# Kernel tuning notes

Measured on AMD Instinct MI355X. Metric: run time of the kernel, lower is better.

The kernel has to match this reference:

```python
import jax, jax.numpy as jnp
import numpy as np
from jax import lax

M = 512      # num_centers
K = 32       # neighbors per center
FEAT = 256   # token feature dim
EPS = 1e-5   # BatchNorm eps


def fps(xyz, m):
    """Furthest point sampling. xyz: (B,N,3) -> idx (B,m) int32."""
    B, N, _ = xyz.shape
    first = jnp.zeros((B,), jnp.int32)

    def step(carry, _):
        min_d, last = carry                       # (B,N), (B,)
        last_pt = jnp.take_along_axis(xyz, last[:, None, None], axis=1)  # (B,1,3)
        d = jnp.sum((xyz - last_pt) ** 2, axis=-1)                       # (B,N)
        min_d = jnp.minimum(min_d, d)
        nxt = jnp.argmax(min_d, axis=1).astype(jnp.int32)
        return (min_d, nxt), nxt

    init = (jnp.full((B, N), 1e10, jnp.float32), first)
    _, rest = lax.scan(step, init, None, length=m - 1)   # (m-1, B)
    return jnp.concatenate([first[None, :], rest], axis=0).T  # (B,m)


def bn(x, g, b, mean, var):
    return (x - mean) * (g * lax.rsqrt(var + EPS)) + b


def setup_inputs() -> dict:
    key = jax.random.key(0)
    ks = jax.random.split(key, 16)
    B, N = 8, 16384
    r = lambda k_, s, sc=0.1: jax.random.normal(k_, s, jnp.float32) * sc
    inp = {
        "xyz": jax.random.normal(ks[0], (B, N, 3), jnp.float32),
        "W1": r(ks[1], (64, 3)), "b1": r(ks[2], (64,)),
        "g1": 1.0 + r(ks[3], (64,)), "be1": r(ks[4], (64,)),
        "m1": r(ks[5], (64,)), "v1": 1.0 + 0.1 * jax.random.uniform(ks[6], (64,)),
        "W2": r(ks[7], (128, 64)), "b2": r(ks[8], (128,)),
        "g2": 1.0 + r(ks[9], (128,)), "be2": r(ks[10], (128,)),
        "m2": r(ks[11], (128,)), "v2": 1.0 + 0.1 * jax.random.uniform(ks[12], (128,)),
        "W3": r(ks[13], (FEAT, 128)), "b3": r(ks[14], (FEAT,)),
        "Wp": r(ks[15], (FEAT, 3)), "bp": jnp.zeros((FEAT,), jnp.float32),
    }
    return inp


def reference(xyz, W1, b1, g1, be1, m1, v1, W2, b2, g2, be2, m2, v2, W3, b3, Wp, bp):
    B, N, _ = xyz.shape
    # --- FPS centers ---
    idx_c = fps(xyz, M)                                            # (B,M)
    centers = jnp.take_along_axis(xyz, idx_c[:, :, None], axis=1)  # (B,M,3)
    # --- brute-force KNN ---
    dist = jnp.sum((centers[:, :, None, :] - xyz[:, None, :, :]) ** 2, axis=-1)  # (B,M,N)
    _, idx = lax.top_k(-dist, K)                                   # (B,M,K)
    nbrs = jnp.take_along_axis(
        xyz, idx.reshape(B, M * K)[:, :, None], axis=1
    ).reshape(B, M, K, 3)
    grouped = nbrs - centers[:, :, None, :]                        # (B,M,K,3)
    # --- MiniPointNet: 1x1 convs == channel matmuls, eval-mode BN ---
    h = jnp.einsum("bmkc,oc->bmko", grouped, W1) + b1
    h = jax.nn.relu(bn(h, g1, be1, m1, v1))
    h = jnp.einsum("bmkc,oc->bmko", h, W2) + b2
    h = jax.nn.relu(bn(h, g2, be2, m2, v2))
    h = jnp.einsum("bmkc,oc->bmko", h, W3) + b3
    tokens = jnp.max(h, axis=2)                                    # (B,M,FEAT)
    pos = jnp.einsum("bmc,oc->bmo", centers, Wp) + bp
    return centers, tokens + pos
```

## Files before the change

### kernel.cpp

```cpp
#include <hip/hip_runtime.h>

typedef unsigned int u32;
typedef unsigned long long u64;
typedef unsigned short u16;

#define DEVFN static __device__ __forceinline__

constexpr int NPTS = 16384;
constexpr int NC = 512;

typedef __attribute__((ext_vector_type(8))) short bf16x8;
typedef __attribute__((ext_vector_type(4))) float f32x4;

#define MFMA16(a, b, c) __builtin_amdgcn_mfma_f32_16x16x32_bf16(a, b, c, 0, 0, 0)

DEVFN u16 bf16rne(float f) {
  u32 b = __float_as_uint(f);
  u32 r = (b + 0x7FFFu + ((b >> 16) & 1u)) >> 16;
  return (u16)r;
}

DEVFN u64 shflx64(u64 v, int m) {
  u32 lo = __shfl_xor((u32)v, m, 64);
  u32 hi = __shfl_xor((u32)(v >> 32), m, 64);
  return ((u64)hi << 32) | lo;
}
DEVFN u64 shfl64(u64 v, int src) {
  u32 lo = __shfl((u32)v, src, 64);
  u32 hi = __shfl((u32)(v >> 32), src, 64);
  return ((u64)hi << 32) | lo;
}

DEVFN void csw(u64& a, u64& b) {
  u64 lo = a < b ? a : b;
  u64 hi = a < b ? b : a;
  a = lo; b = hi;
}

DEVFN u32 spread3(u32 v) {
  return (v & 1u) | ((v & 2u) << 2) | ((v & 4u) << 4) | ((v & 8u) << 6);
}

__global__ __launch_bounds__(1024, 4) void fps_kernel(const float* __restrict__ xyz,
                                                      float* __restrict__ centers) {
  const int b = blockIdx.x;
  const int t = threadIdx.x;
  const int lane = t & 63;
  const int w = t >> 6;
  const float* xb = xyz + (size_t)b * NPTS * 3;

  __shared__ char smem[86016];
  u32* hist = (u32*)smem;
  u16* soidx = (u16*)(smem + 8192);
  u64* skeybuf = (u64*)(smem + 40960);
  float* redB = (float*)(smem + 41216);
  u32* redW = (u32*)(smem + 41664);

  const u32 inf10 = __float_as_uint(1e10f);

  u32 mcode[16];
  {
    float ox[16], oy[16], oz[16];
    float lx = 1e30f, ly = 1e30f, lz = 1e30f;
    float hx = -1e30f, hy = -1e30f, hz = -1e30f;
#pragma unroll
    for (int j = 0; j < 16; ++j) {
      int p = t + j * 1024;
      ox[j] = xb[p * 3 + 0];
      oy[j] = xb[p * 3 + 1];
      oz[j] = xb[p * 3 + 2];
      lx = fminf(lx, ox[j]); hx = fmaxf(hx, ox[j]);
      ly = fminf(ly, oy[j]); hy = fmaxf(hy, oy[j]);
      lz = fminf(lz, oz[j]); hz = fmaxf(hz, oz[j]);
    }
#pragma unroll
    for (int s = 32; s; s >>= 1) {
      lx = fminf(lx, __shfl_xor(lx, s, 64)); hx = fmaxf(hx, __shfl_xor(hx, s, 64));
      ly = fminf(ly, __shfl_xor(ly, s, 64)); hy = fmaxf(hy, __shfl_xor(hy, s, 64));
      lz = fminf(lz, __shfl_xor(lz, s, 64)); hz = fmaxf(hz, __shfl_xor(hz, s, 64));
    }
    if (lane == 0) {
      redB[w * 6 + 0] = lx; redB[w * 6 + 1] = hx;
      redB[w * 6 + 2] = ly; redB[w * 6 + 3] = hy;
      redB[w * 6 + 4] = lz; redB[w * 6 + 5] = hz;
    }
    hist[t] = 0; hist[t + 1024] = 0;
    __syncthreads();
    if (t == 0) {
      float a0 = redB[0], a1 = redB[1], a2 = redB[2], a3 = redB[3], a4 = redB[4], a5 = redB[5];
      for (int q = 1; q < 16; ++q) {
        a0 = fminf(a0, redB[q * 6 + 0]); a1 = fmaxf(a1, redB[q * 6 + 1]);
        a2 = fminf(a2, redB[q * 6 + 2]); a3 = fmaxf(a3, redB[q * 6 + 3]);
        a4 = fminf(a4, redB[q * 6 + 4]); a5 = fmaxf(a5, redB[q * 6 + 5]);
      }
      redB[96] = a0; redB[97] = a1; redB[98] = a2;
      redB[99] = a3; redB[100] = a4; redB[101] = a5;
    }
    __syncthreads();
    const float glx = redB[96], ghx = redB[97];
    const float gly = redB[98], ghy = redB[99];
    const float glz = redB[100], ghz = redB[101];
    const float sx = 15.999f / fmaxf(ghx - glx, 1e-9f);
    const float sy = 15.999f / fmaxf(ghy - gly, 1e-9f);
    const float sz = 7.999f / fmaxf(ghz - glz, 1e-9f);
#pragma unroll
    for (int j = 0; j < 16; ++j) {
      int ix = min(15, max(0, (int)((ox[j] - glx) * sx)));
      int iy = min(15, max(0, (int)((oy[j] - gly) * sy)));
      int iz = min(7, max(0, (int)((oz[j] - glz) * sz)));
      mcode[j] = spread3((u32)ix) | (spread3((u32)iy) << 1) | (spread3((u32)iz) << 2);
    }
  }
#pragma unroll
  for (int j = 0; j < 16; ++j) atomicAdd(&hist[mcode[j]], 1u);
  __syncthreads();
  {
    u32 h0 = hist[t * 2 + 0], h1 = hist[t * 2 + 1];
    u32 s = h0 + h1;
    u32 incl = s;
#pragma unroll
    for (int d = 1; d < 64; d <<= 1) {
      u32 n = __shfl_up(incl, d, 64);
      if (lane >= d) incl += n;
    }
    if (lane == 63) redW[w] = incl;
    __syncthreads();
    if (t == 0) {
      u32 run = 0;
      for (int q = 0; q < 16; ++q) { u32 tmp = redW[q]; redW[q] = run; run += tmp; }
    }
    __syncthreads();
    u32 exc = incl - s + redW[w];
    hist[t * 2 + 0] = exc;
    hist[t * 2 + 1] = exc + h0;
    __syncthreads();
  }
#pragma unroll
  for (int j = 0; j < 16; ++j) {
    u32 p = (u32)(t + j * 1024);
    u32 pos = atomicAdd(&hist[mcode[j]], 1u);
    soidx[pos] = (u16)p;
  }
  __syncthreads();
  const u32 spbase = (u32)((t >> 2) * 64 + (t & 3) * 16);
  float px[16], py[16], pz[16];
  u64 mdkey[16];
#pragma unroll
  for (int j = 0; j < 16; ++j) {
    u32 oidx = (u32)soidx[spbase + j];
    px[j] = xb[oidx * 3 + 0];
    py[j] = xb[oidx * 3 + 1];
    pz[j] = xb[oidx * 3 + 2];
    mdkey[j] = ((u64)inf10 << 32) | (u64)(16383u - oidx);
  }
  float bxl = px[0], bxh = px[0], byl = py[0], byh = py[0], bzl = pz[0], bzh = pz[0];
#pragma unroll
  for (int j = 1; j < 16; ++j) {
    bxl = fminf(bxl, px[j]); bxh = fmaxf(bxh, px[j]);
    byl = fminf(byl, py[j]); byh = fmaxf(byh, py[j]);
    bzl = fminf(bzl, pz[j]); bzh = fmaxf(bzh, pz[j]);
  }
#pragma unroll
  for (int s = 1; s <= 2; s <<= 1) {
    bxl = fminf(bxl, __shfl_xor(bxl, s, 64)); bxh = fmaxf(bxh, __shfl_xor(bxh, s, 64));
    byl = fminf(byl, __shfl_xor(byl, s, 64)); byh = fmaxf(byh, __shfl_xor(byh, s, 64));
    bzl = fminf(bzl, __shfl_xor(bzl, s, 64)); bzh = fmaxf(bzh, __shfl_xor(bzh, s, 64));
  }
  float cx = xb[0], cy = xb[1], cz = xb[2];
  if (t == 0) {
    centers[(b * NC) * 3 + 0] = cx;
    centers[(b * NC) * 3 + 1] = cy;
    centers[(b * NC) * 3 + 2] = cz;
  }
  u64 mdmkey = (u64)inf10 << 32;

  for (int i = 1; i < NC; ++i) {
    float ax = fmaxf(0.f, fmaxf(__fsub_rn(bxl, cx), __fsub_rn(cx, bxh)));
    float ay = fmaxf(0.f, fmaxf(__fsub_rn(byl, cy), __fsub_rn(cy, byh)));
    float az = fmaxf(0.f, fmaxf(__fsub_rn(bzl, cz), __fsub_rn(cz, bzh)));
    float dlb = __fadd_rn(__fadd_rn(__fmul_rn(ax, ax), __fmul_rn(ay, ay)), __fmul_rn(az, az));
    if (dlb < __uint_as_float((u32)(mdmkey >> 32))) {
      u64 lmax = 0ull;
#pragma unroll
      for (int j = 0; j < 16; ++j) {
        float dx = __fsub_rn(px[j], cx);
        float dy = __fsub_rn(py[j], cy);
        float dz = __fsub_rn(pz[j], cz);
        float d = __fadd_rn(__fadd_rn(__fmul_rn(dx, dx), __fmul_rn(dy, dy)), __fmul_rn(dz, dz));
        u64 nk = ((u64)__float_as_uint(d) << 32) | (mdkey[j] & 0xFFFFFFFFull);
        u64 k = nk < mdkey[j] ? nk : mdkey[j];
        mdkey[j] = k;
        lmax = k > lmax ? k : lmax;
      }
      u64 o1 = shflx64(lmax, 1); lmax = o1 > lmax ? o1 : lmax;
      u64 o2 = shflx64(lmax, 2); lmax = o2 > lmax ? o2 : lmax;
      mdmkey = lmax;
    }
    u64 wk = mdmkey;
#pragma unroll
    for (int s = 4; s <= 32; s <<= 1) { u64 o = shflx64(wk, s); wk = o > wk ? o : wk; }
    if (lane == 0) skeybuf[(i & 1) * 16 + w] = wk;
    __syncthreads();
    u64 gk = skeybuf[(i & 1) * 16 + (lane & 15)];
#pragma unroll
    for (int s = 1; s <= 8; s <<= 1) { u64 o = shflx64(gk, s); gk = o > gk ? o : gk; }
    u32 ow = 16383u - (u32)gk;
    ow = __builtin_amdgcn_readfirstlane(ow);
    cx = xb[ow * 3 + 0]; cy = xb[ow * 3 + 1]; cz = xb[ow * 3 + 2];
    if (t == 0) {
      centers[(b * NC + i) * 3 + 0] = cx;
      centers[(b * NC + i) * 3 + 1] = cy;
      centers[(b * NC + i) * 3 + 2] = cz;
    }
  }
}

__global__ __launch_bounds__(512) void knn_kernel(const float* __restrict__ xyz,
                                                  const float* __restrict__ centers,
                                                  float* __restrict__ grouped) {
  __shared__ float spts[1024 * 3];
  __shared__ u64 cand[8][192];
  __shared__ int ccnt[8];
  const int t = threadIdx.x;
  const int lane = t & 63;
  const int w = t >> 6;
  const int cg = blockIdx.x * 8 + w;
  const int b = cg >> 9;
  const float* xb = xyz + (size_t)b * NPTS * 3;
  const float cx = centers[cg * 3 + 0];
  const float cy = centers[cg * 3 + 1];
  const float cz = centers[cg * 3 + 2];
  if (lane == 0) ccnt[w] = 0;

  u64 lmin = ~0ull;
  for (int ch = 0; ch < 16; ++ch) {
    __syncthreads();
    const float* src = xb + ch * 1024 * 3;
#pragma unroll
    for (int q = 0; q < 6; ++q) spts[q * 512 + t] = src[q * 512 + t];
    __syncthreads();
#pragma unroll
    for (int j = 0; j < 16; ++j) {
      int p = lane + j * 64;
      float dx = __fsub_rn(cx, spts[p * 3 + 0]);
      float dy = __fsub_rn(cy, spts[p * 3 + 1]);
      float dz = __fsub_rn(cz, spts[p * 3 + 2]);
      float d = __fadd_rn(__fadd_rn(__fmul_rn(dx, dx), __fmul_rn(dy, dy)), __fmul_rn(dz, dz));
      u64 kk = ((u64)__float_as_uint(d) << 32) | (u64)(u32)(ch * 1024 + p);
      lmin = kk < lmin ? kk : lmin;
    }
  }
  u64 v = lmin;
  for (int k = 2; k <= 64; k <<= 1)
    for (int j = k >> 1; j > 0; j >>= 1) {
      u64 o = shflx64(v, j);
      bool up = ((lane & k) == 0);
      bool lowr = ((lane & j) == 0);
      u64 mn = v < o ? v : o;
      u64 mx = v < o ? o : v;
      v = (lowr == up) ? mn : mx;
    }
  u64 tau = shfl64(v, 31);
  float tf = __uint_as_float((u32)(tau >> 32));

  for (int ch = 0; ch < 16; ++ch) {
    __syncthreads();
    const float* src = xb + ch * 1024 * 3;
#pragma unroll
    for (int q = 0; q < 6; ++q) spts[q * 512 + t] = src[q * 512 + t];
    __syncthreads();
#pragma unroll
    for (int j = 0; j < 16; ++j) {
      int p = lane + j * 64;
      float dx = __fsub_rn(cx, spts[p * 3 + 0]);
      float dy = __fsub_rn(cy, spts[p * 3 + 1]);
      float dz = __fsub_rn(cz, spts[p * 3 + 2]);
      float d = __fadd_rn(__fadd_rn(__fmul_rn(dx, dx), __fmul_rn(dy, dy)), __fmul_rn(dz, dz));
      if (d <= tf) {
        int pos = atomicAdd(&ccnt[w], 1);
        if (pos < 192) cand[w][pos] = ((u64)__float_as_uint(d) << 32) | (u64)(u32)(ch * 1024 + p);
      }
    }
  }
  __syncthreads();
  int cnt = ccnt[w];
  u32 myn = 0u;
  if (cnt <= 192) {
    u64 c0 = (lane < cnt) ? cand[w][lane] : ~0ull;
    u64 c1 = (64 + lane < cnt) ? cand[w][64 + lane] : ~0ull;
    u64 c2 = (128 + lane < cnt) ? cand[w][128 + lane] : ~0ull;
    csw(c0, c1); csw(c1, c2); csw(c0, c1);
    for (int r = 0; r < 32; ++r) {
      u64 wm = c0;
      for (int s = 32; s; s >>= 1) {
        u64 o = shflx64(wm, s);
        wm = o < wm ? o : wm;
      }
      if (c0 == wm) { c0 = c1; c1 = c2; c2 = ~0ull; }
      if (lane == r) myn = (u32)wm;
    }
  } else {
    u64 last = 0ull;
    for (int r = 0; r < 32; ++r) {
      u64 bb = ~0ull;
      for (int j = 0; j < 256; ++j) {
        int p = lane + j * 64;
        float dx = __fsub_rn(cx, xb[p * 3 + 0]);
        float dy = __fsub_rn(cy, xb[p * 3 + 1]);
        float dz = __fsub_rn(cz, xb[p * 3 + 2]);
        float d = __fadd_rn(__fadd_rn(__fmul_rn(dx, dx), __fmul_rn(dy, dy)), __fmul_rn(dz, dz));
        u64 kk = ((u64)__float_as_uint(d) << 32) | (u64)(u32)p;
        if (r == 0 || kk > last)
          if (kk < bb) bb = kk;
      }
      for (int s = 32; s; s >>= 1) {
        u64 o = shflx64(bb, s);
        bb = o < bb ? o : bb;
      }
      last = bb;
      if (lane == r) myn = (u32)bb;
    }
  }
  if (lane < 32) {
    const float nx = xb[(size_t)myn * 3 + 0];
    const float ny = xb[(size_t)myn * 3 + 1];
    const float nz = xb[(size_t)myn * 3 + 2];
    float* gp = grouped + ((size_t)cg * 32 + lane) * 3;
    gp[0] = __fsub_rn(nx, cx);
    gp[1] = __fsub_rn(ny, cy);
    gp[2] = __fsub_rn(nz, cz);
  }
}

__global__ __launch_bounds__(256) void prep_kernel(
    const float* __restrict__ W1, const float* __restrict__ b1,
    const float* __restrict__ g1, const float* __restrict__ be1,
    const float* __restrict__ m1, const float* __restrict__ v1,
    const float* __restrict__ W2, const float* __restrict__ b2,
    const float* __restrict__ g2, const float* __restrict__ be2,
    const float* __restrict__ m2, const float* __restrict__ v2,
    const float* __restrict__ W3,
    float* __restrict__ w1eff, u16* __restrict__ w2L,
    float* __restrict__ t2, u16* __restrict__ w3L) {
  const int tid = blockIdx.x * 256 + threadIdx.x;
  if (tid < 64) {
    float s = g1[tid] / sqrtf(v1[tid] + 1e-5f);
    w1eff[tid * 4 + 0] = W1[tid * 3 + 0] * s;
    w1eff[tid * 4 + 1] = W1[tid * 3 + 1] * s;
    w1eff[tid * 4 + 2] = W1[tid * 3 + 2] * s;
    w1eff[tid * 4 + 3] = (b1[tid] - m1[tid]) * s + be1[tid];
  }
  if (tid < 128) {
    float s = g2[tid] / sqrtf(v2[tid] + 1e-5f);
    t2[tid] = (b2[tid] - m2[tid]) * s + be2[tid];
  }
  if (tid < 8192) {
    int i = tid & 63, o = tid >> 6;
    float s = g2[o] / sqrtf(v2[o] + 1e-5f);
    int kg = i >> 3, j = i & 7;
    w2L[((((kg * 128) + o) * 8) ^ ((kg & 7) * 8)) + j] = bf16rne(W2[o * 64 + i] * s);
  }
  if (tid < 32768) {
    int i = tid & 127, o = tid >> 7;
    int kg = i >> 3, j = i & 7;
    int h = o >> 7, colh = o & 127;
    w3L[h * 16384 + ((((kg * 128) + colh) * 8) ^ ((kg & 7) * 8)) + j] = bf16rne(W3[o * 128 + i]);
  }
}

__global__ __launch_bounds__(256) void mlp_kernel(
    const float* __restrict__ grouped, const u16* __restrict__ w2L,
    const u16* __restrict__ w3L, const float* __restrict__ w1eff,
    const float* __restrict__ t2, const float* __restrict__ b3,
    const float* __restrict__ Wp, const float* __restrict__ bp,
    const float* __restrict__ centers, float* __restrict__ tokens) {
  __shared__ char lds[65536];
  const int t = threadIdx.x;
  const int lane = t & 63;
  const int w = t >> 6;
  const int l15 = lane & 15;
  const int lg = lane >> 4;
  const int c0 = blockIdx.x * 4;
  {
    const u32* s = (const u32*)w2L;
    u32* d = (u32*)lds;
#pragma unroll
    for (int q = 0; q < 16; ++q) d[q * 256 + t] = s[q * 256 + t];
  }
  {
    const int row = t & 127;
    const int oh = (t >> 7) * 32;
    const int cg = c0 + (row >> 5);
    const float* gp = grouped + ((size_t)cg * 32 + (row & 31)) * 3;
    const float gx = gp[0], gy = gp[1], gz = gp[2];
    u16 hv[32];
#pragma unroll
    for (int o = 0; o < 32; ++o) {
      const float4 wvv = ((const float4*)w1eff)[oh + o];
      float h = fmaxf(0.f, gx * wvv.x + gy * wvv.y + gz * wvv.z + wvv.w);
      hv[o] = bf16rne(h);
    }
#pragma unroll
    for (int c4 = 0; c4 < 4; ++c4) {
      uint4 pk;
      pk.x = (u32)hv[c4 * 8 + 0] | ((u32)hv[c4 * 8 + 1] << 16);
      pk.y = (u32)hv[c4 * 8 + 2] | ((u32)hv[c4 * 8 + 3] << 16);
      pk.z = (u32)hv[c4 * 8 + 4] | ((u32)hv[c4 * 8 + 5] << 16);
      pk.w = (u32)hv[c4 * 8 + 6] | ((u32)hv[c4 * 8 + 7] << 16);
      int byte = row * 128 + oh * 2 + c4 * 16;
      *reinterpret_cast<uint4*>(lds + 16384 + (byte ^ ((row & 7) << 4))) = pk;
    }
  }
  __syncthreads();
  f32x4 acc2[2][8];
#pragma unroll
  for (int m = 0; m < 2; ++m)
#pragma unroll
    for (int n = 0; n < 8; ++n) acc2[m][n] = (f32x4){0.f, 0.f, 0.f, 0.f};
#pragma unroll
  for (int ks = 0; ks < 2; ++ks) {
    bf16x8 a[2];
#pragma unroll
    for (int m = 0; m < 2; ++m) {
      int row = w * 32 + m * 16 + l15;
      int byte = row * 128 + (ks * 32 + lg * 8) * 2;
      a[m] = *reinterpret_cast<const bf16x8*>(lds + 16384 + (byte ^ ((row & 7) << 4)));
    }
    const int kg = ks * 4 + lg;
#pragma unroll
    for (int n = 0; n < 8; ++n) {
      int idx = (((kg * 128) + (n * 16 + l15)) * 8) ^ ((kg & 7) * 8);
      bf16x8 bb = *reinterpret_cast<const bf16x8*>((const u16*)lds + idx);
      acc2[0][n] = MFMA16(a[0], bb, acc2[0][n]);
      acc2[1][n] = MFMA16(a[1], bb, acc2[1][n]);
    }
  }
#pragma unroll
  for (int n = 0; n < 8; ++n) {
    const int col = n * 16 + l15;
    const float t2v = t2[col];
#pragma unroll
    for (int m = 0; m < 2; ++m)
#pragma unroll
      for (int r = 0; r < 4; ++r) {
        float vv = fmaxf(0.f, acc2[m][n][r] + t2v);
        int row = w * 32 + m * 16 + lg * 4 + r;
        int byte = row * 256 + col * 2;
        *reinterpret_cast<u16*>(lds + 32768 + (byte ^ ((row & 7) << 4))) = bf16rne(vv);
      }
  }
  __syncthreads();
  const float ccx = centers[(c0 + w) * 3 + 0];
  const float ccy = centers[(c0 + w) * 3 + 1];
  const float ccz = centers[(c0 + w) * 3 + 2];
  float* tok = tokens + (size_t)(c0 + w) * 256;
  for (int h = 0; h < 2; ++h) {
    {
      const u32* s = (const u32*)w3L + h * 8192;
      u32* d = (u32*)lds;
#pragma unroll
      for (int q = 0; q < 32; ++q) d[q * 256 + t] = s[q * 256 + t];
    }
    __syncthreads();
    f32x4 acc3[2][8];
#pragma unroll
    for (int m = 0; m < 2; ++m)
#pragma unroll
      for (int n = 0; n < 8; ++n) acc3[m][n] = (f32x4){0.f, 0.f, 0.f, 0.f};
#pragma unroll
    for (int ks = 0; ks < 4; ++ks) {
      bf16x8 a[2];
#pragma unroll
      for (int m = 0; m < 2; ++m) {
        int row = w * 32 + m * 16 + l15;
        int byte = row * 256 + (ks * 32 + lg * 8) * 2;
        a[m] = *reinterpret_cast<const bf16x8*>(lds + 32768 + (byte ^ ((row & 7) << 4)));
      }
      const int kg = ks * 4 + lg;
#pragma unroll
      for (int n = 0; n < 8; ++n) {
        int idx = (((kg * 128) + (n * 16 + l15)) * 8) ^ ((kg & 7) * 8);
        bf16x8 bb = *reinterpret_cast<const bf16x8*>((const u16*)lds + idx);
        acc3[0][n] = MFMA16(a[0], bb, acc3[0][n]);
        acc3[1][n] = MFMA16(a[1], bb, acc3[1][n]);
      }
    }
#pragma unroll
    for (int n = 0; n < 8; ++n) {
      float vmx = acc3[0][n][0];
#pragma unroll
      for (int m = 0; m < 2; ++m)
#pragma unroll
        for (int r = 0; r < 4; ++r) vmx = fmaxf(vmx, acc3[m][n][r]);
      vmx = fmaxf(vmx, __shfl_xor(vmx, 16, 64));
      vmx = fmaxf(vmx, __shfl_xor(vmx, 32, 64));
      const int col = h * 128 + n * 16 + l15;
      if (lane < 16) {
        float pos = Wp[col * 3 + 0] * ccx + Wp[col * 3 + 1] * ccy +
                    Wp[col * 3 + 2] * ccz + bp[col] + b3[col];
        tok[col] = vmx + pos;
      }
    }
    __syncthreads();
  }
}

extern "C" void kernel_launch(void* const* d_in, const int* in_sizes, int n_in,
                              void* d_out, int out_size, void* d_ws, size_t ws_size,
                              hipStream_t stream) {
  const float* xyz = (const float*)d_in[0];
  const float* W1 = (const float*)d_in[1];
  const float* b1 = (const float*)d_in[2];
  const float* g1 = (const float*)d_in[3];
  const float* be1 = (const float*)d_in[4];
  const float* m1 = (const float*)d_in[5];
  const float* v1 = (const float*)d_in[6];
  const float* W2 = (const float*)d_in[7];
  const float* b2 = (const float*)d_in[8];
  const float* g2 = (const float*)d_in[9];
  const float* be2 = (const float*)d_in[10];
  const float* m2 = (const float*)d_in[11];
  const float* v2 = (const float*)d_in[12];
  const float* W3 = (const float*)d_in[13];
  const float* b3 = (const float*)d_in[14];
  const float* Wp = (const float*)d_in[15];
  const float* bp = (const float*)d_in[16];

  char* ws = (char*)d_ws;
  float* grouped = (float*)ws;
  float* w1eff = (float*)(ws + 1572864);
  u16* w2L = (u16*)(ws + 1573888);
  float* t2 = (float*)(ws + 1590272);
  u16* w3L = (u16*)(ws + 1590784);

  float* centers = (float*)d_out;
  float* tokens = (float*)d_out + 8 * 512 * 3;

  prep_kernel<<<dim3(128), dim3(256), 0, stream>>>(W1, b1, g1, be1, m1, v1,
                                                   W2, b2, g2, be2, m2, v2, W3,
                                                   w1eff, w2L, t2, w3L);
  fps_kernel<<<dim3(8), dim3(1024), 0, stream>>>(xyz, centers);
  knn_kernel<<<dim3(512), dim3(512), 0, stream>>>(xyz, centers, grouped);
  mlp_kernel<<<dim3(1024), dim3(256), 0, stream>>>(grouped, w2L, w3L, w1eff, t2,
                                                   b3, Wp, bp, centers, tokens);
}
```

Baseline: 935.3 us.

## Replace FPS per-iteration reduction with LDS atomicMax and winner-broadcast coordinates

Each wave now finds its local winner and writes that point's coordinates into shared memory. A 64-bit atomicMax on a triple-buffered shared key replaces the second shuffle reduction, and the wave index is packed into the key's low bits so the winning coordinates are read from LDS rather than reloaded from global xyz. Point coordinates move out of registers into a per-thread global workspace, which lowers register pressure, and the occupancy launch bound is dropped. The aim is to shorten the serial per-iteration critical path of 511 steps, at the cost of global/L1 loads inside the distance loop.

```diff
diff --git a/kernel.cpp b/kernel.cpp
--- a/kernel.cpp
+++ b/kernel.cpp
@@ -41,20 +41,21 @@
   return (v & 1u) | ((v & 2u) << 2) | ((v & 4u) << 4) | ((v & 8u) << 6);
 }
 
-__global__ __launch_bounds__(1024, 4) void fps_kernel(const float* __restrict__ xyz,
-                                                      float* __restrict__ centers) {
+__global__ __launch_bounds__(1024) void fps_kernel(const float* __restrict__ xyz,
+                                                   float* __restrict__ centers,
+                                                   float* __restrict__ wsp) {
   const int b = blockIdx.x;
   const int t = threadIdx.x;
   const int lane = t & 63;
   const int w = t >> 6;
   const float* xb = xyz + (size_t)b * NPTS * 3;
 
-  __shared__ char smem[86016];
-  u32* hist = (u32*)smem;
-  u16* soidx = (u16*)(smem + 8192);
-  u64* skeybuf = (u64*)(smem + 40960);
-  float* redB = (float*)(smem + 41216);
-  u32* redW = (u32*)(smem + 41664);
+  __shared__ u32 hist[2048];
+  __shared__ u16 soidx[NPTS];
+  __shared__ u64 gkeybuf[3];
+  __shared__ u32 skb[2][16][4];
+  __shared__ float redB[104];
+  __shared__ u32 redW[16];
 
   const u32 inf10 = __float_as_uint(1e10f);
 
@@ -85,6 +86,7 @@
       redB[w * 6 + 4] = lz; redB[w * 6 + 5] = hz;
     }
     hist[t] = 0; hist[t + 1024] = 0;
+    if (t < 3) gkeybuf[t] = 0ull;
     __syncthreads();
     if (t == 0) {
       float a0 = redB[0], a1 = redB[1], a2 = redB[2], a3 = redB[3], a4 = redB[4], a5 = redB[5];
@@ -143,36 +145,40 @@
   }
   __syncthreads();
   const u32 spbase = (u32)((t >> 2) * 64 + (t & 3) * 16);
-  float px[16], py[16], pz[16];
+  float* wpw = wsp + (size_t)(b * 1024 + t) * 48;
   u64 mdkey[16];
+  u32 lomax = 0;
+  float bxl = 1e30f, bxh = -1e30f, byl = 1e30f, byh = -1e30f, bzl = 1e30f, bzh = -1e30f;
 #pragma unroll
   for (int j = 0; j < 16; ++j) {
     u32 oidx = (u32)soidx[spbase + j];
-    px[j] = xb[oidx * 3 + 0];
-    py[j] = xb[oidx * 3 + 1];
-    pz[j] = xb[oidx * 3 + 2];
-    mdkey[j] = ((u64)inf10 << 32) | (u64)(16383u - oidx);
-  }
-  float bxl = px[0], bxh = px[0], byl = py[0], byh = py[0], bzl = pz[0], bzh = pz[0];
-#pragma unroll
-  for (int j = 1; j < 16; ++j) {
-    bxl = fminf(bxl, px[j]); bxh = fmaxf(bxh, px[j]);
-    byl = fminf(byl, py[j]); byh = fmaxf(byh, py[j]);
-    bzl = fminf(bzl, pz[j]); bzh = fmaxf(bzh, pz[j]);
+    float X = xb[oidx * 3 + 0];
+    float Y = xb[oidx * 3 + 1];
+    float Z = xb[oidx * 3 + 2];
+    wpw[j] = X; wpw[16 + j] = Y; wpw[32 + j] = Z;
+    u32 lo = ((16383u - oidx) << 4) | (u32)w;
+    mdkey[j] = ((u64)inf10 << 32) | lo;
+    lomax = max(lomax, lo);
+    bxl = fminf(bxl, X); bxh = fmaxf(bxh, X);
+    byl = fminf(byl, Y); byh = fmaxf(byh, Y);
+    bzl = fminf(bzl, Z); bzh = fmaxf(bzh, Z);
   }
 #pragma unroll
   for (int s = 1; s <= 2; s <<= 1) {
     bxl = fminf(bxl, __shfl_xor(bxl, s, 64)); bxh = fmaxf(bxh, __shfl_xor(bxh, s, 64));
     byl = fminf(byl, __shfl_xor(byl, s, 64)); byh = fmaxf(byh, __shfl_xor(byh, s, 64));
     bzl = fminf(bzl, __shfl_xor(bzl, s, 64)); bzh = fmaxf(bzh, __shfl_xor(bzh, s, 64));
-  }
+    lomax = max(lomax, (u32)__shfl_xor(lomax, s, 64));
+  }
+  u64 mdmkey = ((u64)inf10 << 32) | lomax;
+  const float* wp = wpw;
+  asm("" : "+v"(wp));
   float cx = xb[0], cy = xb[1], cz = xb[2];
   if (t == 0) {
     centers[(b * NC) * 3 + 0] = cx;
     centers[(b * NC) * 3 + 1] = cy;
     centers[(b * NC) * 3 + 2] = cz;
   }
-  u64 mdmkey = (u64)inf10 << 32;
 
   for (int i = 1; i < NC; ++i) {
     float ax = fmaxf(0.f, fmaxf(__fsub_rn(bxl, cx), __fsub_rn(cx, bxh)));
@@ -183,11 +189,11 @@
       u64 lmax = 0ull;
 #pragma unroll
       for (int j = 0; j < 16; ++j) {
-        float dx = __fsub_rn(px[j], cx);
-        float dy = __fsub_rn(py[j], cy);
-        float dz = __fsub_rn(pz[j], cz);
+        float dx = __fsub_rn(wp[j], cx);
+        float dy = __fsub_rn(wp[16 + j], cy);
+        float dz = __fsub_rn(wp[32 + j], cz);
         float d = __fadd_rn(__fadd_rn(__fmul_rn(dx, dx), __fmul_rn(dy, dy)), __fmul_rn(dz, dz));
-        u64 nk = ((u64)__float_as_uint(d) << 32) | (mdkey[j] & 0xFFFFFFFFull);
+        u64 nk = ((u64)__float_as_uint(d) << 32) | (u64)(u32)mdkey[j];
         u64 k = nk < mdkey[j] ? nk : mdkey[j];
         mdkey[j] = k;
         lmax = k > lmax ? k : lmax;
@@ -199,14 +205,22 @@
     u64 wk = mdmkey;
 #pragma unroll
     for (int s = 4; s <= 32; s <<= 1) { u64 o = shflx64(wk, s); wk = o > wk ? o : wk; }
-    if (lane == 0) skeybuf[(i & 1) * 16 + w] = wk;
-    __syncthreads();
-    u64 gk = skeybuf[(i & 1) * 16 + (lane & 15)];
-#pragma unroll
-    for (int s = 1; s <= 8; s <<= 1) { u64 o = shflx64(gk, s); gk = o > gk ? o : gk; }
-    u32 ow = 16383u - (u32)gk;
-    ow = __builtin_amdgcn_readfirstlane(ow);
-    cx = xb[ow * 3 + 0]; cy = xb[ow * 3 + 1]; cz = xb[ow * 3 + 2];
+#pragma unroll
+    for (int j = 0; j < 16; ++j) {
+      if (mdkey[j] == wk) {
+        skb[i & 1][w][0] = __float_as_uint(wp[j]);
+        skb[i & 1][w][1] = __float_as_uint(wp[16 + j]);
+        skb[i & 1][w][2] = __float_as_uint(wp[32 + j]);
+      }
+    }
+    if (t == 0) gkeybuf[(i + 1) % 3] = 0ull;
+    if (lane == 0) atomicMax((u64*)&gkeybuf[i % 3], wk);
+    __syncthreads();
+    u64 g = gkeybuf[i % 3];
+    u32 widx = (u32)g & 15u;
+    cx = __uint_as_float(skb[i & 1][widx][0]);
+    cy = __uint_as_float(skb[i & 1][widx][1]);
+    cz = __uint_as_float(skb[i & 1][widx][2]);
     if (t == 0) {
       centers[(b * NC + i) * 3 + 0] = cx;
       centers[(b * NC + i) * 3 + 1] = cy;
@@ -532,6 +546,7 @@
   u16* w2L = (u16*)(ws + 1573888);
   float* t2 = (float*)(ws + 1590272);
   u16* w3L = (u16*)(ws + 1590784);
+  float* wsp = (float*)(ws + 1656320);
 
   float* centers = (float*)d_out;
   float* tokens = (float*)d_out + 8 * 512 * 3;
@@ -539,7 +554,7 @@
   prep_kernel<<<dim3(128), dim3(256), 0, stream>>>(W1, b1, g1, be1, m1, v1,
                                                    W2, b2, g2, be2, m2, v2, W3,
                                                    w1eff, w2L, t2, w3L);
-  fps_kernel<<<dim3(8), dim3(1024), 0, stream>>>(xyz, centers);
+  fps_kernel<<<dim3(8), dim3(1024), 0, stream>>>(xyz, centers, wsp);
   knn_kernel<<<dim3(512), dim3(512), 0, stream>>>(xyz, centers, grouped);
   mlp_kernel<<<dim3(1024), dim3(256), 0, stream>>>(grouped, w2L, w3L, w1eff, t2,
                                                    b3, Wp, bp, centers, tokens);
```

Result: slower. 1.188 ms (+27.0%).
